# Kernel optimization log

Measured on AMD Instinct MI355X. Metric: run time of the kernel, lower is better.

Reference implementation:

```python
import jax, jax.numpy as jnp
import numpy as np

B, S, HID = 1, 2048, 4096
H, HKV, D = 32, 8, 128
GROUPS = H // HKV
ROPE_BASE = 10000.0


def setup_inputs() -> dict:
    key = jax.random.key(0)
    k1, k2, k3, k4, k5 = jax.random.split(key, 5)
    s = 0.02
    return {
        "hidden_states": jax.random.normal(k1, (B, S, HID), dtype=jnp.float32),
        "Wq": jax.random.normal(k2, (H * D, HID), dtype=jnp.float32) * s,
        "Wk": jax.random.normal(k3, (HKV * D, HID), dtype=jnp.float32) * s,
        "Wv": jax.random.normal(k4, (HKV * D, HID), dtype=jnp.float32) * s,
        "Wo": jax.random.normal(k5, (HID, H * D), dtype=jnp.float32) * s,
    }


def _rotate_half(x):
    x1, x2 = x[..., : D // 2], x[..., D // 2 :]
    return jnp.concatenate((-x2, x1), axis=-1)


def _rope_tables(seq_len):
    inv_freq = 1.0 / (ROPE_BASE ** (jnp.arange(0, D, 2, dtype=jnp.float32) / D))
    t = jnp.arange(seq_len, dtype=jnp.float32)
    freqs = jnp.outer(t, inv_freq)            # [S, D/2]
    emb = jnp.concatenate((freqs, freqs), -1)  # [S, D]
    return jnp.cos(emb)[None, None], jnp.sin(emb)[None, None]  # [1,1,S,D]


def reference(hidden_states, Wq, Wk, Wv, Wo):
    b, s, _ = hidden_states.shape
    scale = D ** -0.5
    q = (hidden_states @ Wq.T).reshape(b, s, H, D).transpose(0, 2, 1, 3)    # [B,H,S,D]
    k = (hidden_states @ Wk.T).reshape(b, s, HKV, D).transpose(0, 2, 1, 3)  # [B,HKV,S,D]
    v = (hidden_states @ Wv.T).reshape(b, s, HKV, D).transpose(0, 2, 1, 3)

    cos, sin = _rope_tables(s)
    q = q * cos + _rotate_half(q) * sin
    k = k * cos + _rotate_half(k) * sin

    # repeat_kv: h = kv_h * groups + g -> consecutive repeat along head axis
    k_rep = jnp.repeat(k, GROUPS, axis=1)  # [B,H,S,D]
    v_rep = jnp.repeat(v, GROUPS, axis=1)

    scores = jnp.einsum("bhqd,bhkd->bhqk", q, k_rep) * scale
    causal = jnp.tril(jnp.ones((s, s), dtype=bool))
    scores = jnp.where(causal[None, None], scores, jnp.finfo(scores.dtype).min)
    probs = jax.nn.softmax(scores, axis=-1)
    attn = jnp.einsum("bhqk,bhkd->bhqd", probs, v_rep)  # [B,H,S,D]
    attn = attn.transpose(0, 2, 1, 3).reshape(b, s, H * D)
    return attn @ Wo.T
```

## Files before the change

### kernel.cpp

```cpp
#include <hip/hip_runtime.h>

#define AS1 __attribute__((address_space(1)))
#define AS3 __attribute__((address_space(3)))

typedef __bf16 bf16;
typedef __bf16 bf16x8 __attribute__((ext_vector_type(8)));
typedef float f32x4 __attribute__((ext_vector_type(4)));

__device__ __forceinline__ void gld_lds16(const bf16* g, bf16* l) {
    __builtin_amdgcn_global_load_lds((const AS1 void*)g, (AS3 void*)l, 16, 0, 0);
}

#define SB0 __builtin_amdgcn_sched_barrier(0)

__global__ void cvt_all_kernel(const float4* __restrict__ h, const float4* __restrict__ wq,
                               const float4* __restrict__ wk, const float4* __restrict__ wv,
                               const float4* __restrict__ wo, ushort4* __restrict__ hs,
                               ushort4* __restrict__ wb) {
    for (int i = blockIdx.x * 256 + threadIdx.x; i < 12582912; i += 2048 * 256) {
        const float4* src;
        ushort4* dst;
        if (i < 2097152)      { src = h  + i;             dst = hs + i; }
        else if (i < 6291456) { src = wq + (i - 2097152); dst = wb + (i - 2097152); }
        else if (i < 7340032) { src = wk + (i - 6291456); dst = wb + 4194304 + (i - 6291456); }
        else if (i < 8388608) { src = wv + (i - 7340032); dst = wb + 5242880 + (i - 7340032); }
        else                  { src = wo + (i - 8388608); dst = wb + 6291456 + (i - 8388608); }
        const float4 v = *src;
        ushort4 r;
        r.x = __builtin_bit_cast(unsigned short, (bf16)v.x);
        r.y = __builtin_bit_cast(unsigned short, (bf16)v.y);
        r.z = __builtin_bit_cast(unsigned short, (bf16)v.z);
        r.w = __builtin_bit_cast(unsigned short, (bf16)v.w);
        *dst = r;
    }
}

template <int BN, bool OUTF32>
__launch_bounds__(512, 2)
__global__ void gemm8p_kernel(const bf16* __restrict__ A, const bf16* __restrict__ W,
                              void* __restrict__ Cout, int M, int N, int K) {
    constexpr int NF = BN / 64;
    constexpr int IB = BN / 128;
    __shared__ __align__(16) bf16 Asl[4][128 * 32];
    __shared__ __align__(16) bf16 Bsl[4][BN * 32];

    const int tn = blockIdx.x * BN;
    const int tm = blockIdx.y * 128;
    const int tid = threadIdx.x;
    const int wave = tid >> 6;
    const int lane = tid & 63;
    const int laneR = lane & 15;
    const int laneS = lane >> 4;
    const int wmB = (wave >> 2) * 64;
    const int wnB = (wave & 3) * (BN / 4);
    const int NT = K >> 5;
    const int sofs = (laneS ^ ((laneR >> 1) & 3)) << 3;

    auto stage = [&](int t) {
        const int slot = t & 3;
        const int k0 = t << 5;
        {
            const int row = tid >> 2, g = tid & 3;
            const int sg = g ^ ((row >> 1) & 3);
            gld_lds16(A + (size_t)(tm + row) * K + k0 + sg * 8, &Asl[slot][wave * 512]);
        }
#pragma unroll
        for (int i = 0; i < IB; ++i) {
            const int row = i * 128 + (tid >> 2), g = tid & 3;
            const int sg = g ^ ((row >> 1) & 3);
            gld_lds16(W + (size_t)(tn + row) * K + k0 + sg * 8,
                      &Bsl[slot][i * 4096 + wave * 512]);
        }
    };

    f32x4 acc[4][NF] = {};

    stage(0); stage(1); stage(2);
    if constexpr (BN == 384) asm volatile("s_waitcnt vmcnt(8)" ::: "memory");
    else                     asm volatile("s_waitcnt vmcnt(6)" ::: "memory");
    SB0;
    __builtin_amdgcn_s_barrier();
    SB0;

    for (int t = 0; t < NT; ++t) {
        const int slot = t & 3;
        bf16x8 af[4], bfr[NF];
#pragma unroll
        for (int mf = 0; mf < 4; ++mf)
            af[mf] = *(const bf16x8*)&Asl[slot][(wmB + mf * 16 + laneR) * 32 + sofs];
#pragma unroll
        for (int nf = 0; nf < NF; ++nf)
            bfr[nf] = *(const bf16x8*)&Bsl[slot][(wnB + nf * 16 + laneR) * 32 + sofs];

        if (t + 3 < NT) stage(t + 3);

#pragma unroll
        for (int mf = 0; mf < 4; ++mf)
#pragma unroll
            for (int nf = 0; nf < NF; ++nf)
                acc[mf][nf] = __builtin_amdgcn_mfma_f32_16x16x32_bf16(af[mf], bfr[nf], acc[mf][nf], 0, 0, 0);

        SB0;
        if (t + 3 < NT) {
            if constexpr (BN == 384) asm volatile("s_waitcnt vmcnt(8)" ::: "memory");
            else                     asm volatile("s_waitcnt vmcnt(6)" ::: "memory");
        } else if (t + 3 == NT) {
            if constexpr (BN == 384) asm volatile("s_waitcnt vmcnt(4)" ::: "memory");
            else                     asm volatile("s_waitcnt vmcnt(3)" ::: "memory");
        } else {
            asm volatile("s_waitcnt vmcnt(0)" ::: "memory");
        }
        SB0;
        __builtin_amdgcn_s_barrier();
        SB0;
    }

    const int rbase = laneS * 4;
#pragma unroll
    for (int mf = 0; mf < 4; ++mf)
#pragma unroll
        for (int nf = 0; nf < NF; ++nf)
#pragma unroll
            for (int rr = 0; rr < 4; ++rr) {
                const size_t row = (size_t)tm + wmB + mf * 16 + rbase + rr;
                const size_t col = (size_t)tn + wnB + nf * 16 + laneR;
                if constexpr (OUTF32) ((float*)Cout)[row * N + col] = acc[mf][nf][rr];
                else                  ((bf16*)Cout)[row * N + col] = (bf16)acc[mf][nf][rr];
            }
    (void)M;
}

__global__ void rope_table_kernel(float* __restrict__ ct, float* __restrict__ st) {
    const int idx = blockIdx.x * 256 + threadIdx.x;
    const int f = idx & 63;
    const int s = idx >> 6;
    const float th = s * expf(-0.14391156831212787f * (float)f);
    ct[idx] = cosf(th);
    st[idx] = sinf(th);
}

__global__ void rope_tv_kernel(const bf16* __restrict__ C, bf16* __restrict__ Qr,
                               bf16* __restrict__ Kr, bf16* __restrict__ Vt,
                               const float* __restrict__ ct, const float* __restrict__ st) {
    __shared__ __align__(16) unsigned short tbuf[64][136];
    const int bid = blockIdx.x;
    const int tid = threadIdx.x;
    if (bid < 20480) {
        const int idx = bid * 256 + tid;
        const int NQ = 2048 * 32 * 64;
        const float QSC = 0.12751743561884394f;
        if (idx < NQ) {
            const int f = idx & 63;
            const int t = idx >> 6;
            const int h = t & 31;
            const int s = t >> 5;
            const float x1 = (float)C[(size_t)s * 6144 + h * 128 + f];
            const float x2 = (float)C[(size_t)s * 6144 + h * 128 + f + 64];
            const float cs = ct[(s << 6) + f], sn = st[(s << 6) + f];
            bf16* dst = Qr + ((size_t)h * 2048 + s) * 128 + f;
            dst[0]  = (bf16)((x1 * cs - x2 * sn) * QSC);
            dst[64] = (bf16)((x2 * cs + x1 * sn) * QSC);
        } else {
            const int i2 = idx - NQ;
            const int f = i2 & 63;
            const int t = i2 >> 6;
            const int h = t & 7;
            const int s = t >> 3;
            const float x1 = (float)C[(size_t)s * 6144 + 4096 + h * 128 + f];
            const float x2 = (float)C[(size_t)s * 6144 + 4096 + h * 128 + f + 64];
            const float cs = ct[(s << 6) + f], sn = st[(s << 6) + f];
            bf16* dst = Kr + ((size_t)h * 2048 + s) * 128 + f;
            dst[0]  = (bf16)(x1 * cs - x2 * sn);
            dst[64] = (bf16)(x2 * cs + x1 * sn);
        }
    } else {
        const int b2 = bid - 20480;
        const int hkv = b2 >> 5;
        const int st8 = b2 & 31;
        const int s0 = st8 * 64;
#pragma unroll
        for (int it = 0; it < 4; ++it) {
            const int l = it * 2048 + tid * 8;
            const int r = l >> 7, c = l & 127;
            *(bf16x8*)&tbuf[r][c] = *(const bf16x8*)&C[(size_t)(s0 + r) * 6144 + 5120 + hkv * 128 + c];
        }
        __syncthreads();
#pragma unroll
        for (int it = 0; it < 8; ++it) {
            const int o = it * 1024 + tid * 4;
            const int d = o >> 6, j = o & 63;
            ushort4 pk;
            pk.x = tbuf[j + 0][d];
            pk.y = tbuf[j + 1][d];
            pk.z = tbuf[j + 2][d];
            pk.w = tbuf[j + 3][d];
            *(ushort4*)&Vt[((size_t)hkv * 128 + d) * 2048 + s0 + j] = pk;
        }
    }
}

__launch_bounds__(512, 1)
__global__ void flash_attn_kernel(const bf16* __restrict__ Qr, const bf16* __restrict__ Kr,
                                  const bf16* __restrict__ Vt, bf16* __restrict__ Aout) {
    __shared__ __align__(16) bf16 Klds[2][128 * 128];
    __shared__ __align__(16) bf16 Vlds[2][128 * 128];
    __shared__ __align__(16) char Plds[8][2048];

    const int bid = blockIdx.x;
    const int hkv = bid & 7;
    const int r = bid >> 3;
    const int h = hkv * 4 + (r & 3);
    const int pa = r >> 2;
    const int qbA = 15 - pa, qbB = pa;
    const int tid = threadIdx.x;
    const int wave = tid >> 6, lane = tid & 63;
    const int laneR = lane & 15;
    const int laneS = lane >> 4;
    const int laneK = laneS * 8;
    const int rbase = laneS * 4;

    const bf16* Kh = Kr + (size_t)hkv * 2048 * 128;
    const bf16* Vh = Vt + (size_t)hkv * 128 * 2048;
    char* Pw = Plds[wave];

    auto stageK = [&](int kv0, int buf) {
#pragma unroll
        for (int s = 0; s < 4; ++s) {
            const int chunk = wave * 4 + s;
            const int L = chunk * 64 + lane;
            const int row = L >> 4, sl = L & 15;
            gld_lds16(Kh + (size_t)(kv0 + row) * 128 + ((sl ^ (row & 7)) << 3),
                      &Klds[buf][chunk * 512]);
        }
    };
    auto stageV = [&](int kv0, int buf) {
#pragma unroll
        for (int s = 0; s < 4; ++s) {
            const int chunk = wave * 4 + s;
            const int L = chunk * 64 + lane;
            const int row = L >> 4, sl = L & 15;
            gld_lds16(Vh + (size_t)row * 2048 + kv0 + ((sl ^ (row & 7)) << 3),
                      &Vlds[buf][chunk * 512]);
        }
    };

    int qbcur = qbA;
    int q0w = qbA * 128 + wave * 16;
    int tloc = 0;

    bf16x8 qf[4];
    auto loadQ = [&]() {
#pragma unroll
        for (int kc = 0; kc < 4; ++kc)
            qf[kc] = *(const bf16x8*)&Qr[((size_t)h * 2048 + q0w + laneR) * 128 + kc * 32 + laneK];
    };
    loadQ();

    f32x4 o[8] = {};
    float mrow[4], lrow[4];
#pragma unroll
    for (int rr = 0; rr < 4; ++rr) { mrow[rr] = -1e30f; lrow[rr] = 0.f; }

    stageK(0, 0);
    stageV(0, 0);
    __syncthreads();

    for (int g = 0; g < 17; ++g) {
        const int buf = g & 1;
        if (g < 16) {
            const int tn = (g + 1 <= qbA) ? (g + 1) : (g - qbA);
            stageK(tn * 128, buf ^ 1);
            stageV(tn * 128, buf ^ 1);
        }
        const int kv0 = tloc * 128;

        f32x4 sc[8] = {};
        __builtin_amdgcn_s_setprio(1);
#pragma unroll
        for (int kc = 0; kc < 4; ++kc) {
            bf16x8 kf[8];
#pragma unroll
            for (int j = 0; j < 8; ++j) {
                const int row = j * 16 + laneR;
                kf[j] = *(const bf16x8*)((const char*)Klds[buf] + row * 256 +
                                         ((kc * 64 + laneS * 16) ^ ((row & 7) << 4)));
            }
#pragma unroll
            for (int j = 0; j < 8; ++j)
                sc[j] = __builtin_amdgcn_mfma_f32_16x16x32_bf16(qf[kc], kf[j], sc[j], 0, 0, 0);
        }
        __builtin_amdgcn_s_setprio(0);

        if (tloc == qbcur) {
#pragma unroll
            for (int j = 0; j < 8; ++j)
#pragma unroll
                for (int rr = 0; rr < 4; ++rr) {
                    const int qr = q0w + rbase + rr;
                    const int kr = kv0 + j * 16 + laneR;
                    if (kr > qr) sc[j][rr] = -1e30f;
                }
        }

#pragma unroll
        for (int rr = 0; rr < 4; ++rr) {
            float v = sc[0][rr];
#pragma unroll
            for (int j = 1; j < 8; ++j) v = fmaxf(v, sc[j][rr]);
            v = fmaxf(v, __shfl_xor(v, 1, 64));
            v = fmaxf(v, __shfl_xor(v, 2, 64));
            v = fmaxf(v, __shfl_xor(v, 4, 64));
            v = fmaxf(v, __shfl_xor(v, 8, 64));
            float m0 = mrow[rr];
            if (v - m0 > 8.0f) {
                const float fac = __builtin_exp2f(m0 - v);
                mrow[rr] = v;
                m0 = v;
                lrow[rr] *= fac;
#pragma unroll
                for (int j = 0; j < 8; ++j) o[j][rr] *= fac;
            }
            float rs = 0.f;
#pragma unroll
            for (int j = 0; j < 8; ++j) {
                const float p = __builtin_exp2f(sc[j][rr] - m0);
                sc[j][rr] = p;
                rs += p;
            }
            rs += __shfl_xor(rs, 1, 64);
            rs += __shfl_xor(rs, 2, 64);
            rs += __shfl_xor(rs, 4, 64);
            rs += __shfl_xor(rs, 8, 64);
            lrow[rr] += rs;
        }

#pragma unroll
        for (int hf = 0; hf < 2; ++hf) {
#pragma unroll
            for (int j = 0; j < 4; ++j)
#pragma unroll
                for (int rr = 0; rr < 4; ++rr) {
                    const int row = rbase + rr;
                    *(bf16*)(Pw + row * 128 + ((j * 32 + laneR * 2) ^ ((row & 7) << 4))) =
                        (bf16)sc[hf * 4 + j][rr];
                }
            __builtin_amdgcn_s_setprio(1);
#pragma unroll
            for (int kc = 0; kc < 2; ++kc) {
                bf16x8 pf = *(const bf16x8*)(Pw + laneR * 128 +
                                             ((kc * 64 + laneS * 16) ^ ((laneR & 7) << 4)));
                const int kcg = hf * 2 + kc;
                bf16x8 vf[8];
#pragma unroll
                for (int j = 0; j < 8; ++j) {
                    const int row = j * 16 + laneR;
                    vf[j] = *(const bf16x8*)((const char*)Vlds[buf] + row * 256 +
                                             ((kcg * 64 + laneS * 16) ^ ((row & 7) << 4)));
                }
#pragma unroll
                for (int j = 0; j < 8; ++j)
                    o[j] = __builtin_amdgcn_mfma_f32_16x16x32_bf16(pf, vf[j], o[j], 0, 0, 0);
            }
            __builtin_amdgcn_s_setprio(0);
        }

        if (tloc == qbcur) {
            float rinv[4];
#pragma unroll
            for (int rr = 0; rr < 4; ++rr) rinv[rr] = 1.0f / lrow[rr];
#pragma unroll
            for (int j = 0; j < 8; ++j)
#pragma unroll
                for (int rr = 0; rr < 4; ++rr) {
                    const size_t row = (size_t)q0w + rbase + rr;
                    Aout[row * 4096 + h * 128 + j * 16 + laneR] = (bf16)(o[j][rr] * rinv[rr]);
                }
            if (g < 16) {
                qbcur = qbB;
                q0w = qbB * 128 + wave * 16;
                tloc = 0;
                loadQ();
#pragma unroll
                for (int rr = 0; rr < 4; ++rr) { mrow[rr] = -1e30f; lrow[rr] = 0.f; }
#pragma unroll
                for (int j = 0; j < 8; ++j) o[j] = f32x4{0.f, 0.f, 0.f, 0.f};
            }
        } else {
            ++tloc;
        }

        __syncthreads();
    }
}

extern "C" void kernel_launch(void* const* d_in, const int* in_sizes, int n_in,
                              void* d_out, int out_size, void* d_ws, size_t ws_size,
                              hipStream_t stream) {
    const float* hidden = (const float*)d_in[0];
    const float* Wq = (const float*)d_in[1];
    const float* Wk = (const float*)d_in[2];
    const float* Wv = (const float*)d_in[3];
    const float* Wo = (const float*)d_in[4];
    float* out = (float*)d_out;
    char* ws = (char*)d_ws;

    bf16* hs = (bf16*)(ws + 0);
    bf16* Wb = (bf16*)(ws + 16777216);
    bf16* Cq = (bf16*)(ws + 100663296);
    bf16* Qr = (bf16*)(ws + 125829120);
    bf16* Kr = (bf16*)(ws + 142606336);
    bf16* Vt = (bf16*)(ws + 146800640);
    bf16* At = (bf16*)(ws + 150994944);
    float* ct = (float*)(ws + 0);
    float* st = (float*)(ws + 524288);
    (void)ws_size; (void)in_sizes; (void)n_in; (void)out_size;

    cvt_all_kernel<<<2048, 256, 0, stream>>>((const float4*)hidden, (const float4*)Wq,
                                             (const float4*)Wk, (const float4*)Wv,
                                             (const float4*)Wo, (ushort4*)hs, (ushort4*)Wb);

    gemm8p_kernel<384, false><<<dim3(16, 16), 512, 0, stream>>>(hs, Wb, Cq, 2048, 6144, 4096);

    rope_table_kernel<<<512, 256, 0, stream>>>(ct, st);
    rope_tv_kernel<<<20736, 256, 0, stream>>>(Cq, Qr, Kr, Vt, ct, st);

    flash_attn_kernel<<<256, 512, 0, stream>>>(Qr, Kr, Vt, At);

    gemm8p_kernel<256, true><<<dim3(16, 16), 512, 0, stream>>>(At, Wb + 25165824, out, 2048, 4096, 4096);
}
```

Before: 319.1 us.

## Fuse RoPE, Q scaling and V transpose into QKV GEMM epilogue

Adds a dedicated QKV GEMM whose epilogue stages the output tile in LDS, then applies RoPE and the Q scale and writes Qr/Kr, or writes V transposed, directly. This removes the intermediate Cq buffer round-trip and the separate rope/transpose kernel launch. The rope table computation is folded into the conversion kernel. The epilogue uses scalar global stores and a 128KB LDS buffer, which may limit occupancy and store efficiency.

```diff
diff --git a/kernel.cpp b/kernel.cpp
--- a/kernel.cpp
+++ b/kernel.cpp
@@ -16,7 +16,8 @@
 __global__ void cvt_all_kernel(const float4* __restrict__ h, const float4* __restrict__ wq,
                                const float4* __restrict__ wk, const float4* __restrict__ wv,
                                const float4* __restrict__ wo, ushort4* __restrict__ hs,
-                               ushort4* __restrict__ wb) {
+                               ushort4* __restrict__ wb, float* __restrict__ ct,
+                               float* __restrict__ st) {
     for (int i = blockIdx.x * 256 + threadIdx.x; i < 12582912; i += 2048 * 256) {
         const float4* src;
         ushort4* dst;
@@ -33,6 +34,138 @@
         r.w = __builtin_bit_cast(unsigned short, (bf16)v.w);
         *dst = r;
     }
+    if (blockIdx.x < 512) {
+        const int idx = blockIdx.x * 256 + threadIdx.x;
+        const int f = idx & 63;
+        const int s = idx >> 6;
+        const float th = s * expf(-0.14391156831212787f * (float)f);
+        ct[idx] = cosf(th);
+        st[idx] = sinf(th);
+    }
+}
+
+__launch_bounds__(512, 2)
+__global__ void gemm_qkv_kernel(const bf16* __restrict__ A, const bf16* __restrict__ W,
+                                bf16* __restrict__ Qr, bf16* __restrict__ Kr,
+                                bf16* __restrict__ Vt, const float* __restrict__ ct,
+                                const float* __restrict__ st, int K) {
+    __shared__ __align__(16) char smem[131072];
+    bf16* AslB = (bf16*)smem;
+    bf16* BslB = (bf16*)(smem + 32768);
+    bf16* LDSe = (bf16*)smem;
+
+    const int tn = blockIdx.x * 384;
+    const int tm = blockIdx.y * 128;
+    const int tid = threadIdx.x;
+    const int wave = tid >> 6;
+    const int lane = tid & 63;
+    const int laneR = lane & 15;
+    const int laneS = lane >> 4;
+    const int wmB = (wave >> 2) * 64;
+    const int wnB = (wave & 3) * 96;
+    const int NT = K >> 5;
+    const int sofs = (laneS ^ ((laneR >> 1) & 3)) << 3;
+
+    auto stage = [&](int t) {
+        const int slot = t & 3;
+        const int k0 = t << 5;
+        {
+            const int row = tid >> 2, g = tid & 3;
+            const int sg = g ^ ((row >> 1) & 3);
+            gld_lds16(A + (size_t)(tm + row) * K + k0 + sg * 8, AslB + slot * 4096 + wave * 512);
+        }
+#pragma unroll
+        for (int i = 0; i < 3; ++i) {
+            const int row = i * 128 + (tid >> 2), g = tid & 3;
+            const int sg = g ^ ((row >> 1) & 3);
+            gld_lds16(W + (size_t)(tn + row) * K + k0 + sg * 8,
+                      BslB + slot * 12288 + i * 4096 + wave * 512);
+        }
+    };
+
+    f32x4 acc[4][6] = {};
+
+    stage(0); stage(1); stage(2);
+    asm volatile("s_waitcnt vmcnt(8)" ::: "memory");
+    SB0;
+    __builtin_amdgcn_s_barrier();
+    SB0;
+
+    for (int t = 0; t < NT; ++t) {
+        const int slot = t & 3;
+        bf16x8 af[4], bfr[6];
+#pragma unroll
+        for (int mf = 0; mf < 4; ++mf)
+            af[mf] = *(const bf16x8*)(AslB + slot * 4096 + (wmB + mf * 16 + laneR) * 32 + sofs);
+#pragma unroll
+        for (int nf = 0; nf < 6; ++nf)
+            bfr[nf] = *(const bf16x8*)(BslB + slot * 12288 + (wnB + nf * 16 + laneR) * 32 + sofs);
+
+        if (t + 3 < NT) stage(t + 3);
+
+#pragma unroll
+        for (int mf = 0; mf < 4; ++mf)
+#pragma unroll
+            for (int nf = 0; nf < 6; ++nf)
+                acc[mf][nf] = __builtin_amdgcn_mfma_f32_16x16x32_bf16(af[mf], bfr[nf], acc[mf][nf], 0, 0, 0);
+
+        SB0;
+        if (t + 3 < NT)       asm volatile("s_waitcnt vmcnt(8)" ::: "memory");
+        else if (t + 3 == NT) asm volatile("s_waitcnt vmcnt(4)" ::: "memory");
+        else                  asm volatile("s_waitcnt vmcnt(0)" ::: "memory");
+        SB0;
+        __builtin_amdgcn_s_barrier();
+        SB0;
+    }
+
+    const int rbase = laneS * 4;
+#pragma unroll
+    for (int mf = 0; mf < 4; ++mf)
+#pragma unroll
+        for (int nf = 0; nf < 6; ++nf)
+#pragma unroll
+            for (int rr = 0; rr < 4; ++rr) {
+                const int row = wmB + mf * 16 + rbase + rr;
+                const int col = wnB + nf * 16 + laneR;
+                LDSe[row * 386 + col] = (bf16)acc[mf][nf][rr];
+            }
+    __syncthreads();
+
+    const float QSC = 0.12751743561884394f;
+    const int nqk = min(max(5120 - tn, 0), 384);
+    const int nqkb = nqk >> 7;
+    for (int it = 0; it < nqkb * 16; ++it) {
+        const int g = it * 512 + tid;
+        const int f = g & 63;
+        const int row = (g >> 6) & 127;
+        const int blk = g >> 13;
+        const int c = tn + blk * 128;
+        const float x1 = (float)LDSe[row * 386 + blk * 128 + f];
+        const float x2 = (float)LDSe[row * 386 + blk * 128 + f + 64];
+        const int s = tm + row;
+        const float cs = ct[(s << 6) + f], sn = st[(s << 6) + f];
+        const float o1 = x1 * cs - x2 * sn;
+        const float o2 = x2 * cs + x1 * sn;
+        if (c < 4096) {
+            bf16* dst = Qr + ((size_t)(c >> 7) * 2048 + s) * 128 + f;
+            dst[0]  = (bf16)(o1 * QSC);
+            dst[64] = (bf16)(o2 * QSC);
+        } else {
+            bf16* dst = Kr + ((size_t)((c - 4096) >> 7) * 2048 + s) * 128 + f;
+            dst[0]  = (bf16)o1;
+            dst[64] = (bf16)o2;
+        }
+    }
+
+    const int nv = 384 - nqk;
+    for (int it = 0; it < (nv >> 2); ++it) {
+        const int g = it * 512 + tid;
+        const int row = g & 127;
+        const int cv = g >> 7;
+        const int dv = tn + nqk + cv - 5120;
+        Vt[((size_t)(dv >> 7) * 128 + (dv & 127)) * 2048 + tm + row] =
+            LDSe[row * 386 + nqk + cv];
+    }
 }
 
 template <int BN, bool OUTF32>
@@ -128,75 +261,6 @@
                 else                  ((bf16*)Cout)[row * N + col] = (bf16)acc[mf][nf][rr];
             }
     (void)M;
-}
-
-__global__ void rope_table_kernel(float* __restrict__ ct, float* __restrict__ st) {
-    const int idx = blockIdx.x * 256 + threadIdx.x;
-    const int f = idx & 63;
-    const int s = idx >> 6;
-    const float th = s * expf(-0.14391156831212787f * (float)f);
-    ct[idx] = cosf(th);
-    st[idx] = sinf(th);
-}
-
-__global__ void rope_tv_kernel(const bf16* __restrict__ C, bf16* __restrict__ Qr,
-                               bf16* __restrict__ Kr, bf16* __restrict__ Vt,
-                               const float* __restrict__ ct, const float* __restrict__ st) {
-    __shared__ __align__(16) unsigned short tbuf[64][136];
-    const int bid = blockIdx.x;
-    const int tid = threadIdx.x;
-    if (bid < 20480) {
-        const int idx = bid * 256 + tid;
-        const int NQ = 2048 * 32 * 64;
-        const float QSC = 0.12751743561884394f;
-        if (idx < NQ) {
-            const int f = idx & 63;
-            const int t = idx >> 6;
-            const int h = t & 31;
-            const int s = t >> 5;
-            const float x1 = (float)C[(size_t)s * 6144 + h * 128 + f];
-            const float x2 = (float)C[(size_t)s * 6144 + h * 128 + f + 64];
-            const float cs = ct[(s << 6) + f], sn = st[(s << 6) + f];
-            bf16* dst = Qr + ((size_t)h * 2048 + s) * 128 + f;
-            dst[0]  = (bf16)((x1 * cs - x2 * sn) * QSC);
-            dst[64] = (bf16)((x2 * cs + x1 * sn) * QSC);
-        } else {
-            const int i2 = idx - NQ;
-            const int f = i2 & 63;
-            const int t = i2 >> 6;
-            const int h = t & 7;
-            const int s = t >> 3;
-            const float x1 = (float)C[(size_t)s * 6144 + 4096 + h * 128 + f];
-            const float x2 = (float)C[(size_t)s * 6144 + 4096 + h * 128 + f + 64];
-            const float cs = ct[(s << 6) + f], sn = st[(s << 6) + f];
-            bf16* dst = Kr + ((size_t)h * 2048 + s) * 128 + f;
-            dst[0]  = (bf16)(x1 * cs - x2 * sn);
-            dst[64] = (bf16)(x2 * cs + x1 * sn);
-        }
-    } else {
-        const int b2 = bid - 20480;
-        const int hkv = b2 >> 5;
-        const int st8 = b2 & 31;
-        const int s0 = st8 * 64;
-#pragma unroll
-        for (int it = 0; it < 4; ++it) {
-            const int l = it * 2048 + tid * 8;
-            const int r = l >> 7, c = l & 127;
-            *(bf16x8*)&tbuf[r][c] = *(const bf16x8*)&C[(size_t)(s0 + r) * 6144 + 5120 + hkv * 128 + c];
-        }
-        __syncthreads();
-#pragma unroll
-        for (int it = 0; it < 8; ++it) {
-            const int o = it * 1024 + tid * 4;
-            const int d = o >> 6, j = o & 63;
-            ushort4 pk;
-            pk.x = tbuf[j + 0][d];
-            pk.y = tbuf[j + 1][d];
-            pk.z = tbuf[j + 2][d];
-            pk.w = tbuf[j + 3][d];
-            *(ushort4*)&Vt[((size_t)hkv * 128 + d) * 2048 + s0 + j] = pk;
-        }
-    }
 }
 
 __launch_bounds__(512, 1)
@@ -406,23 +470,20 @@
 
     bf16* hs = (bf16*)(ws + 0);
     bf16* Wb = (bf16*)(ws + 16777216);
-    bf16* Cq = (bf16*)(ws + 100663296);
+    float* ct = (float*)(ws + 100663296);
+    float* st = (float*)(ws + 101187584);
     bf16* Qr = (bf16*)(ws + 125829120);
     bf16* Kr = (bf16*)(ws + 142606336);
     bf16* Vt = (bf16*)(ws + 146800640);
     bf16* At = (bf16*)(ws + 150994944);
-    float* ct = (float*)(ws + 0);
-    float* st = (float*)(ws + 524288);
     (void)ws_size; (void)in_sizes; (void)n_in; (void)out_size;
 
     cvt_all_kernel<<<2048, 256, 0, stream>>>((const float4*)hidden, (const float4*)Wq,
                                              (const float4*)Wk, (const float4*)Wv,
-                                             (const float4*)Wo, (ushort4*)hs, (ushort4*)Wb);
-
-    gemm8p_kernel<384, false><<<dim3(16, 16), 512, 0, stream>>>(hs, Wb, Cq, 2048, 6144, 4096);
-
-    rope_table_kernel<<<512, 256, 0, stream>>>(ct, st);
-    rope_tv_kernel<<<20736, 256, 0, stream>>>(Cq, Qr, Kr, Vt, ct, st);
+                                             (const float4*)Wo, (ushort4*)hs, (ushort4*)Wb,
+                                             ct, st);
+
+    gemm_qkv_kernel<<<dim3(16, 16), 512, 0, stream>>>(hs, Wb, Qr, Kr, Vt, ct, st, 4096);
 
     flash_attn_kernel<<<256, 512, 0, stream>>>(Qr, Kr, Vt, At);
 
```

Result: faster. 308.0 us (-3.5%).
